# Optimization experiments

Hardware: AMD Instinct MI355X
Metric: run time of the kernel (lower is better)

The kernel has to match this reference:

```python
import jax, jax.numpy as jnp
import numpy as np

D = 1024   # dim_model
H = 16     # num_heads
DH = D // H  # per-head dim for k and v
B, S = 2, 2048
EPS = 1e-5


def layer_norm(x, g, b):
    mu = jnp.mean(x, axis=-1, keepdims=True)
    var = jnp.var(x, axis=-1, keepdims=True)
    return (x - mu) * jax.lax.rsqrt(var + EPS) * g + b


def setup_inputs() -> dict:
    key = jax.random.key(0)
    ks = jax.random.split(key, 8)
    s_d = 1.0 / np.sqrt(D)
    inp = {
        "x": jax.random.normal(ks[0], (B, S, D), dtype=jnp.float32),
        # stacked per-head projections, [H, D, DH] (torch Linear weight.T per head)
        "wq": jax.random.uniform(ks[1], (H, D, DH), jnp.float32, -s_d, s_d),
        "wk": jax.random.uniform(ks[2], (H, D, DH), jnp.float32, -s_d, s_d),
        "wv": jax.random.uniform(ks[3], (H, D, DH), jnp.float32, -s_d, s_d),
        "wo": jax.random.uniform(ks[4], (D, D), jnp.float32, -s_d, s_d),
        "w1": jax.random.uniform(ks[5], (D, D), jnp.float32, -s_d, s_d),  # FFN hidden == dim_model per source
        "w2": jax.random.uniform(ks[6], (D, D), jnp.float32, -s_d, s_d),
        "ln1_g": jnp.ones((D,), jnp.float32), "ln1_b": jnp.zeros((D,), jnp.float32),
        "ln2_g": jnp.ones((D,), jnp.float32), "ln2_b": jnp.zeros((D,), jnp.float32),
        "ln3_g": jnp.ones((D,), jnp.float32), "ln3_b": jnp.zeros((D,), jnp.float32),
    }
    return inp


def reference(x, wq, wk, wv, wo, w1, w2, ln1_g, ln1_b, ln2_g, ln2_b, ln3_g, ln3_b):
    residual = x
    h = layer_norm(x, ln1_g, ln1_b)  # pre_attention_norm
    # batched multi-head attention (equivalent to per-head loop + concat)
    q = jnp.einsum("bsd,hdk->bhsk", h, wq)
    k = jnp.einsum("bsd,hdk->bhsk", h, wk)
    v = jnp.einsum("bsd,hdk->bhsk", h, wv)
    scores = jnp.einsum("bhsk,bhtk->bhst", q, k) / jnp.sqrt(jnp.float32(DH))
    attn = jax.nn.softmax(scores, axis=-1)
    ctx = jnp.einsum("bhst,bhtk->bhsk", attn, v)        # [B,H,S,DH]
    concat = ctx.transpose(0, 2, 1, 3).reshape(x.shape[0], x.shape[1], -1)  # head concat order
    h = concat @ wo
    h = h + residual
    h = layer_norm(h, ln2_g, ln2_b)  # post_attention_norm (dropout is identity, rate=0)
    residual = h
    ffn = jnp.maximum(h @ w1, 0.0) @ w2
    h = ffn + residual
    h = layer_norm(h, ln3_g, ln3_b)  # post_ffn_norm
    return h
```

## Files before the change

kernel.cpp:

```cpp
#include <hip/hip_runtime.h>
#include <stdint.h>

typedef unsigned short u16;
typedef __attribute__((ext_vector_type(8))) short short8;
typedef __attribute__((ext_vector_type(4))) short short4v;
typedef __attribute__((ext_vector_type(4))) float f32x4;

#define DEV static __device__ __forceinline__

constexpr int DMODEL = 1024;
constexpr int SEQ = 2048;

DEV u16 f2b(float f){
  uint32_t u = __float_as_uint(f);
  u += 0x7FFF + ((u >> 16) & 1);
  return (u16)(u >> 16);
}

DEV float b2f(u16 b){ uint32_t u = ((uint32_t)b)<<16; return __uint_as_float(u); }

#define AS1(p) ((const __attribute__((address_space(1))) void*)(p))
#define AS3(p) ((__attribute__((address_space(3))) void*)(p))
#define GLOAD_LDS16(g, l) __builtin_amdgcn_global_load_lds(AS1(g), AS3(l), 16, 0, 0)
#define LDSADDR(p) ((uint32_t)(size_t)((__attribute__((address_space(3))) void*)(p)))

DEV short4v ds_tr16(uint32_t a){
  short4v r;
  asm volatile("ds_read_b64_tr_b16 %0, %1" : "=v"(r) : "v"(a) : "memory");
  return r;
}

DEV void pswap(uint32_t &a, uint32_t &b){
  asm("v_permlane32_swap_b32 %0, %1":"+v"(a),"+v"(b));
  asm("v_permlane16_swap_b32 %0, %1":"+v"(a),"+v"(b));
}

DEV uint32_t cvtpk(float lo, float hi){
  uint32_t r; asm("v_cvt_pk_bf16_f32 %0, %1, %2":"=v"(r):"v"(lo),"v"(hi)); return r;
}

__global__ __launch_bounds__(256) void transpose_all(
    const float* __restrict__ wq, const float* __restrict__ wk,
    const float* __restrict__ wv, const float* __restrict__ wo,
    const float* __restrict__ w1, const float* __restrict__ w2,
    u16* __restrict__ WqkvT, u16* __restrict__ WoT,
    u16* __restrict__ W1T, u16* __restrict__ W2T){
  __shared__ float tile[64][65];
  int bid = blockIdx.x;
  int j = threadIdx.x & 63, i0 = threadIdx.x >> 6;
  if(bid < 768){
    int xb = bid & 15, z = bid >> 4;
    int p = z >> 4, h = z & 15;
    const float* src = (p==0?wq:(p==1?wk:wv)) + (size_t)h*1024*64;
    float sc = (p==0) ? 0.18033688011112042f : 1.0f;
    int r0 = xb*64;
    for(int i=i0;i<64;i+=4) tile[i][j] = src[(size_t)(r0+i)*64 + j];
    __syncthreads();
    u16* drow = WqkvT + ((size_t)p*1024 + h*64)*1024;
    for(int jj=i0;jj<64;jj+=4) drow[(size_t)jj*1024 + r0 + j] = f2b(tile[j][jj]*sc);
  } else {
    int t = bid - 768;
    int which = t >> 8; t &= 255;
    const float* src = which==0?wo:(which==1?w1:w2);
    u16* dst = which==0?WoT:(which==1?W1T:W2T);
    int r0 = (t&15)*64, c0 = (t>>4)*64;
    for(int i=i0;i<64;i+=4) tile[i][j] = src[(size_t)(r0+i)*1024 + c0 + j];
    __syncthreads();
    for(int jj=i0;jj<64;jj+=4) dst[(size_t)(c0+jj)*1024 + r0 + j] = f2b(tile[j][jj]);
  }
}

__global__ __launch_bounds__(256) void ln_kernel(
    const float* __restrict__ in, const float* __restrict__ g, const float* __restrict__ bb,
    u16* __restrict__ outb, float* __restrict__ outf){
  int row = blockIdx.x, tid = threadIdx.x;
  const float4* x4 = (const float4*)(in + (size_t)row*DMODEL);
  float4 v = x4[tid];
  float s  = v.x+v.y+v.z+v.w;
  float ss = v.x*v.x + v.y*v.y + v.z*v.z + v.w*v.w;
  #pragma unroll
  for(int m=1;m<64;m<<=1){ s += __shfl_xor(s,m); ss += __shfl_xor(ss,m); }
  __shared__ float red[8];
  int w = tid>>6;
  if((tid&63)==0){ red[w]=s; red[4+w]=ss; }
  __syncthreads();
  s  = red[0]+red[1]+red[2]+red[3];
  ss = red[4]+red[5]+red[6]+red[7];
  float mu  = s*(1.f/DMODEL);
  float var = ss*(1.f/DMODEL) - mu*mu;
  float rs  = rsqrtf(var + 1e-5f);
  float4 gv = ((const float4*)g)[tid];
  float4 bv = ((const float4*)bb)[tid];
  float y0=(v.x-mu)*rs*gv.x+bv.x, y1=(v.y-mu)*rs*gv.y+bv.y;
  float y2=(v.z-mu)*rs*gv.z+bv.z, y3=(v.w-mu)*rs*gv.w+bv.w;
  if(outb){ ushort4 o = make_ushort4(f2b(y0),f2b(y1),f2b(y2),f2b(y3));
            ((ushort4*)outb)[(size_t)row*(DMODEL/4) + tid] = o; }
  if(outf){ ((float4*)outf)[(size_t)row*(DMODEL/4) + tid] = make_float4(y0,y1,y2,y3); }
}

__global__ __launch_bounds__(256) void ln_kernel_bf(
    const u16* __restrict__ in, const float* __restrict__ g, const float* __restrict__ bb,
    u16* __restrict__ outb, float* __restrict__ outf){
  int row = blockIdx.x, tid = threadIdx.x;
  ushort4 vb = ((const ushort4*)(in + (size_t)row*DMODEL))[tid];
  float v0=b2f(vb.x), v1=b2f(vb.y), v2=b2f(vb.z), v3=b2f(vb.w);
  float s  = v0+v1+v2+v3;
  float ss = v0*v0 + v1*v1 + v2*v2 + v3*v3;
  #pragma unroll
  for(int m=1;m<64;m<<=1){ s += __shfl_xor(s,m); ss += __shfl_xor(ss,m); }
  __shared__ float red[8];
  int w = tid>>6;
  if((tid&63)==0){ red[w]=s; red[4+w]=ss; }
  __syncthreads();
  s  = red[0]+red[1]+red[2]+red[3];
  ss = red[4]+red[5]+red[6]+red[7];
  float mu  = s*(1.f/DMODEL);
  float var = ss*(1.f/DMODEL) - mu*mu;
  float rs  = rsqrtf(var + 1e-5f);
  float4 gv = ((const float4*)g)[tid];
  float4 bv = ((const float4*)bb)[tid];
  float y0=(v0-mu)*rs*gv.x+bv.x, y1=(v1-mu)*rs*gv.y+bv.y;
  float y2=(v2-mu)*rs*gv.z+bv.z, y3=(v3-mu)*rs*gv.w+bv.w;
  if(outb){ ushort4 o = make_ushort4(f2b(y0),f2b(y1),f2b(y2),f2b(y3));
            ((ushort4*)outb)[(size_t)row*(DMODEL/4) + tid] = o; }
  if(outf){ ((float4*)outf)[(size_t)row*(DMODEL/4) + tid] = make_float4(y0,y1,y2,y3); }
}

template<int MODE>
__global__ __launch_bounds__(256) void gemm_bt(
    const u16* __restrict__ A, const u16* __restrict__ BT, int M, int N, int K,
    float* __restrict__ outf, u16* __restrict__ outb, const float* __restrict__ resf,
    const u16* __restrict__ resb,
    u16* __restrict__ oq, u16* __restrict__ ok, u16* __restrict__ ov){
  __shared__ u16 lsA[2][4096];
  __shared__ u16 lsB[2][4096];
  int n0 = blockIdx.x*128, m0 = blockIdx.y*128;
  int tid = threadIdx.x, lane = tid&63, w = tid>>6;
  int wr = w>>1, wc = w&1, rq = lane&15, hk = lane>>4;
  int o0 = tid*16, o1 = 4096 + tid*16;
  const u16* aS0 = A  + (size_t)(m0 + (o0>>6))*K + ((o0&63)>>1);
  const u16* aS1 = A  + (size_t)(m0 + (o1>>6))*K + ((o1&63)>>1);
  const u16* bS0 = BT + (size_t)(n0 + (o0>>6))*K + ((o0&63)>>1);
  const u16* bS1 = BT + (size_t)(n0 + (o1>>6))*K + ((o1&63)>>1);
  int nk = K>>5;
  f32x4 acc[4][4] = {};
  GLOAD_LDS16(aS0, &lsA[0][w*512]);
  GLOAD_LDS16(aS1, &lsA[0][2048 + w*512]);
  GLOAD_LDS16(bS0, &lsB[0][w*512]);
  GLOAD_LDS16(bS1, &lsB[0][2048 + w*512]);
  #pragma unroll 2
  for(int kt=0; kt<nk; ++kt){
    __syncthreads();
    if(kt+1 < nk){
      int nb = (kt+1)&1;
      GLOAD_LDS16(aS0 + (kt+1)*32, &lsA[nb][w*512]);
      GLOAD_LDS16(aS1 + (kt+1)*32, &lsA[nb][2048 + w*512]);
      GLOAD_LDS16(bS0 + (kt+1)*32, &lsB[nb][w*512]);
      GLOAD_LDS16(bS1 + (kt+1)*32, &lsB[nb][2048 + w*512]);
    }
    const u16* la = &lsA[kt&1][0];
    const u16* lb = &lsB[kt&1][0];
    short8 aF[4], bF[4];
    #pragma unroll
    for(int m=0;m<4;++m) aF[m] = *(const short8*)(la + (wr*64 + m*16 + rq)*32 + hk*8);
    #pragma unroll
    for(int n=0;n<4;++n) bF[n] = *(const short8*)(lb + (wc*64 + n*16 + rq)*32 + hk*8);
    __builtin_amdgcn_s_setprio(1);
    #pragma unroll
    for(int m=0;m<4;++m){
      #pragma unroll
      for(int n=0;n<4;++n)
        acc[m][n] = __builtin_amdgcn_mfma_f32_16x16x32_bf16(aF[m], bF[n], acc[m][n], 0,0,0);
    }
    __builtin_amdgcn_s_setprio(0);
  }
  #pragma unroll
  for(int m=0;m<4;++m){
    #pragma unroll
    for(int n=0;n<4;++n){
      int rb = m0 + wr*64 + m*16 + (hk<<2);
      int c  = n0 + wc*64 + n*16 + rq;
      #pragma unroll
      for(int qq=0;qq<4;++qq){
        int r = rb+qq; float val = acc[m][n][qq];
        if constexpr(MODE==1){
          int proj=c>>10, n1=c&1023, h=n1>>6, d2=n1&63;
          int b=r>>11, si=r&2047;
          u16* dst = proj==0?oq:(proj==1?ok:ov);
          dst[(((size_t)(b*16+h))*SEQ + si)*64 + d2] = f2b(val);
        } else if constexpr(MODE==2){
          outf[(size_t)r*N + c] = val + resf[(size_t)r*N + c];
        } else if constexpr(MODE==3){
          outb[(size_t)r*N + c] = f2b(val>0.f?val:0.f);
        } else if constexpr(MODE==4){
          outf[(size_t)r*N + c] = val + b2f(resb[(size_t)r*N + c]);
        } else if constexpr(MODE==5){
          outb[(size_t)r*N + c] = f2b(val + resf[(size_t)r*N + c]);
        } else if constexpr(MODE==6){
          outb[(size_t)r*N + c] = f2b(val + b2f(resb[(size_t)r*N + c]));
        } else {
          outb[(size_t)r*N + c] = f2b(val);
        }
      }
    }
  }
}

__global__ __launch_bounds__(256) void attn_kernel(
    const u16* __restrict__ q, const u16* __restrict__ k, const u16* __restrict__ v,
    u16* __restrict__ concat){
  __shared__ u16 lsK[2][4096];
  __shared__ u16 lsV[2][4096];
  int qt = blockIdx.x, bh = blockIdx.y;
  const u16* qp = q + (size_t)bh*SEQ*64;
  const u16* kp = k + (size_t)bh*SEQ*64;
  const u16* vp = v + (size_t)bh*SEQ*64;
  int tid=threadIdx.x, lane=tid&63, w=tid>>6;
  int rq = lane&15, hk = lane>>4;
  const uint32_t sw = (uint32_t)((rq&7)<<4);

  short8 aQ[2];
  {
    const u16* qrow = qp + (size_t)(qt*64 + w*16 + rq)*64 + hk*8;
    aQ[0] = *(const short8*)(qrow);
    aQ[1] = *(const short8*)(qrow + 32);
  }
  short8 bOnes;
  #pragma unroll
  for(int j=0;j<8;++j) bOnes[j] = (short)0x3F80;

  int o0 = tid*16,        kr0 = o0>>7;
  int o1 = 4096 + tid*16, kr1 = o1>>7;
  int koff0 = kr0*64 + ((((o0&127) ^ ((kr0&7)<<4)))>>1);
  int koff1 = kr1*64 + ((((o1&127) ^ ((kr1&7)<<4)))>>1);
  auto vdec = [](int c)->int{
    int t  = ((c>>5)<<2) | ((c&7)>>1);
    int d8 = (((c>>3)&3)<<1) | (c&1);
    return t*64 + d8*8;
  };
  int voff0 = vdec(tid), voff1 = vdec(256+tid);

  f32x4 accO[4] = {};
  f32x4 accL = {};

  GLOAD_LDS16(kp + koff0, &lsK[0][0   + w*512]);
  GLOAD_LDS16(kp + koff1, &lsK[0][2048+ w*512]);
  GLOAD_LDS16(vp + voff0, &lsV[0][0   + w*512]);
  GLOAD_LDS16(vp + voff1, &lsV[0][2048+ w*512]);

  int cur = 0;
  for(int kt=0; kt<SEQ/64; ++kt){
    __syncthreads();
    if(kt+1 < SEQ/64){
      int b = cur^1;
      const u16* ksrc = kp + (kt+1)*4096;
      const u16* vsrc = vp + (kt+1)*4096;
      GLOAD_LDS16(ksrc + koff0, &lsK[b][0   + w*512]);
      GLOAD_LDS16(ksrc + koff1, &lsK[b][2048+ w*512]);
      GLOAD_LDS16(vsrc + voff0, &lsV[b][0   + w*512]);
      GLOAD_LDS16(vsrc + voff1, &lsV[b][2048+ w*512]);
    }
    const char* kb = (const char*)&lsK[cur][0];
    short8 bK[4][2];
    #pragma unroll
    for(int ts=0;ts<4;++ts){
      uint32_t rb = (uint32_t)((ts*16+rq)*128);
      bK[ts][0] = *(const short8*)(kb + rb + (((uint32_t)(hk<<4)) ^ sw));
      bK[ts][1] = *(const short8*)(kb + rb + ((64u|(uint32_t)(hk<<4)) ^ sw));
    }
    f32x4 z[4];
    __builtin_amdgcn_s_setprio(1);
    #pragma unroll
    for(int ts=0;ts<4;++ts){
      f32x4 zz = {};
      zz = __builtin_amdgcn_mfma_f32_16x16x32_bf16(bK[ts][0], aQ[0], zz, 0,0,0);
      zz = __builtin_amdgcn_mfma_f32_16x16x32_bf16(bK[ts][1], aQ[1], zz, 0,0,0);
      z[ts] = zz;
    }
    __builtin_amdgcn_s_setprio(0);
    uint32_t vA = LDSADDR(&lsV[cur][0]) + (uint32_t)(hk*1024 + rq*2);
    short4v vL[2][4][2];
    #pragma unroll
    for(int kh=0;kh<2;++kh){
      #pragma unroll
      for(int ds=0;ds<4;++ds){
        vL[kh][ds][0] = ds_tr16(vA + kh*4096 + ds*128);
        vL[kh][ds][1] = ds_tr16(vA + kh*4096 + ds*128 + 512);
      }
    }
    #pragma unroll
    for(int ts=0;ts<4;++ts){
      #pragma unroll
      for(int r=0;r<4;++r)
        z[ts][r] = __builtin_exp2f(z[ts][r]);
    }
    uint32_t u00=cvtpk(z[0][0],z[0][1]), u01=cvtpk(z[0][2],z[0][3]);
    uint32_t u10=cvtpk(z[1][0],z[1][1]), u11=cvtpk(z[1][2],z[1][3]);
    uint32_t u20=cvtpk(z[2][0],z[2][1]), u21=cvtpk(z[2][2],z[2][3]);
    uint32_t u30=cvtpk(z[3][0],z[3][1]), u31=cvtpk(z[3][2],z[3][3]);
    pswap(u00,u10); pswap(u01,u11);
    pswap(u20,u30); pswap(u21,u31);
    union U8 { uint32_t d[4]; short8 v; } ap0, ap1;
    ap0.d[0]=u00; ap0.d[1]=u01; ap0.d[2]=u10; ap0.d[3]=u11;
    ap1.d[0]=u20; ap1.d[1]=u21; ap1.d[2]=u30; ap1.d[3]=u31;
    asm volatile("s_waitcnt lgkmcnt(0)" ::: "memory");
    __builtin_amdgcn_sched_barrier(0);
    __builtin_amdgcn_s_setprio(1);
    #pragma unroll
    for(int kh=0;kh<2;++kh){
      short8 aP = kh ? ap1.v : ap0.v;
      accL = __builtin_amdgcn_mfma_f32_16x16x32_bf16(aP, bOnes, accL, 0,0,0);
      #pragma unroll
      for(int ds=0;ds<4;++ds){
        short8 bV = __builtin_shufflevector(vL[kh][ds][0], vL[kh][ds][1], 0,1,2,3,4,5,6,7);
        accO[ds] = __builtin_amdgcn_mfma_f32_16x16x32_bf16(aP, bV, accO[ds], 0,0,0);
      }
    }
    __builtin_amdgcn_s_setprio(0);
    cur ^= 1;
  }
  int b = bh>>4, h = bh&15;
  #pragma unroll
  for(int r=0;r<4;++r){
    float inv = 1.f / accL[r];
    int si = qt*64 + w*16 + hk*4 + r;
    #pragma unroll
    for(int ds=0;ds<4;++ds){
      int c = h*64 + ds*16 + rq;
      concat[((size_t)b*SEQ + si)*DMODEL + c] = f2b(accO[ds][r] * inv);
    }
  }
}

extern "C" void kernel_launch(void* const* d_in, const int* in_sizes, int n_in,
                              void* d_out, int out_size, void* d_ws, size_t ws_size,
                              hipStream_t stream){
  (void)in_sizes; (void)n_in; (void)out_size; (void)ws_size;
  const float* x    = (const float*)d_in[0];
  const float* wq   = (const float*)d_in[1];
  const float* wk   = (const float*)d_in[2];
  const float* wv   = (const float*)d_in[3];
  const float* wo   = (const float*)d_in[4];
  const float* w1   = (const float*)d_in[5];
  const float* w2   = (const float*)d_in[6];
  const float* ln1g = (const float*)d_in[7];
  const float* ln1b = (const float*)d_in[8];
  const float* ln2g = (const float*)d_in[9];
  const float* ln2b = (const float*)d_in[10];
  const float* ln3g = (const float*)d_in[11];
  const float* ln3b = (const float*)d_in[12];
  float* out = (float*)d_out;

  char* ws = (char*)d_ws; size_t off = 0;
  auto alloc = [&](size_t b)->char*{ char* p = ws + off; off += (b + 255) & ~(size_t)255; return p; };
  u16*   WqkvT = (u16*)  alloc((size_t)3072*1024*2);
  u16*   WoT   = (u16*)  alloc((size_t)1024*1024*2);
  u16*   W1T   = (u16*)  alloc((size_t)1024*1024*2);
  u16*   W2T   = (u16*)  alloc((size_t)1024*1024*2);
  u16*   h1    = (u16*)  alloc((size_t)4096*1024*2);
  u16*   qb    = (u16*)  alloc((size_t)4194304*2);
  u16*   kb    = (u16*)  alloc((size_t)4194304*2);
  u16*   vb    = (u16*)  alloc((size_t)4194304*2);
  u16*   cc    = (u16*)  alloc((size_t)4096*1024*2);
  u16*   r1b   = (u16*)  alloc((size_t)4096*1024*2);
  u16*   h2b   = (u16*)  alloc((size_t)4096*1024*2);
  u16*   r2b   = (u16*)  alloc((size_t)4096*1024*2);
  u16*   ffn1  = h1;

  transpose_all<<<1536,256,0,stream>>>(wq,wk,wv,wo,w1,w2, WqkvT,WoT,W1T,W2T);

  ln_kernel<<<4096,256,0,stream>>>(x, ln1g, ln1b, h1, nullptr);
  gemm_bt<1><<<dim3(24,32),256,0,stream>>>(h1,WqkvT,4096,3072,1024,
      nullptr,nullptr,nullptr,nullptr, qb,kb,vb);
  attn_kernel<<<dim3(32,32),256,0,stream>>>(qb,kb,vb,cc);
  gemm_bt<5><<<dim3(8,32),256,0,stream>>>(cc,WoT,4096,1024,1024,
      nullptr,r1b,x,nullptr, nullptr,nullptr,nullptr);
  ln_kernel_bf<<<4096,256,0,stream>>>(r1b, ln2g, ln2b, h2b, nullptr);
  gemm_bt<3><<<dim3(8,32),256,0,stream>>>(h2b,W1T,4096,1024,1024,
      nullptr,ffn1,nullptr,nullptr, nullptr,nullptr,nullptr);
  gemm_bt<6><<<dim3(8,32),256,0,stream>>>(ffn1,W2T,4096,1024,1024,
      nullptr,r2b,nullptr,h2b, nullptr,nullptr,nullptr);
  ln_kernel_bf<<<4096,256,0,stream>>>(r2b, ln3g, ln3b, nullptr, out);
}
```

Baseline: 203.9 us.

## Double attention block query tile to 128 rows with 512 threads sharing K/V tiles

The attention kernel now runs 8 waves per block, each handling 16 query rows, so one block covers 128 queries instead of 64. Each shared K/V tile in LDS now serves twice as many queries, and each thread issues one global-to-LDS load per tensor instead of two. This halves K/V global traffic and halves the grid size. The cost is fewer blocks (512) and more waves waiting at each barrier, which could lower occupancy or add synchronisation stalls.

```diff
diff --git a/kernel.cpp b/kernel.cpp
--- a/kernel.cpp
+++ b/kernel.cpp
@@ -206,7 +206,7 @@
   }
 }
 
-__global__ __launch_bounds__(256) void attn_kernel(
+__global__ __launch_bounds__(512) void attn_kernel(
     const u16* __restrict__ q, const u16* __restrict__ k, const u16* __restrict__ v,
     u16* __restrict__ concat){
   __shared__ u16 lsK[2][4096];
@@ -221,7 +221,7 @@
 
   short8 aQ[2];
   {
-    const u16* qrow = qp + (size_t)(qt*64 + w*16 + rq)*64 + hk*8;
+    const u16* qrow = qp + (size_t)(qt*128 + w*16 + rq)*64 + hk*8;
     aQ[0] = *(const short8*)(qrow);
     aQ[1] = *(const short8*)(qrow + 32);
   }
@@ -229,36 +229,25 @@
   #pragma unroll
   for(int j=0;j<8;++j) bOnes[j] = (short)0x3F80;
 
-  int o0 = tid*16,        kr0 = o0>>7;
-  int o1 = 4096 + tid*16, kr1 = o1>>7;
-  int koff0 = kr0*64 + ((((o0&127) ^ ((kr0&7)<<4)))>>1);
-  int koff1 = kr1*64 + ((((o1&127) ^ ((kr1&7)<<4)))>>1);
-  auto vdec = [](int c)->int{
-    int t  = ((c>>5)<<2) | ((c&7)>>1);
-    int d8 = (((c>>3)&3)<<1) | (c&1);
-    return t*64 + d8*8;
-  };
-  int voff0 = vdec(tid), voff1 = vdec(256+tid);
+  int o = tid*16, kr = o>>7;
+  int koff = kr*64 + ((((o&127) ^ ((kr&7)<<4)))>>1);
+  int vt  = ((tid>>5)<<2) | ((tid&7)>>1);
+  int vd8 = (((tid>>3)&3)<<1) | (tid&1);
+  int voff = vt*64 + vd8*8;
 
   f32x4 accO[4] = {};
   f32x4 accL = {};
 
-  GLOAD_LDS16(kp + koff0, &lsK[0][0   + w*512]);
-  GLOAD_LDS16(kp + koff1, &lsK[0][2048+ w*512]);
-  GLOAD_LDS16(vp + voff0, &lsV[0][0   + w*512]);
-  GLOAD_LDS16(vp + voff1, &lsV[0][2048+ w*512]);
+  GLOAD_LDS16(kp + koff, &lsK[0][w*512]);
+  GLOAD_LDS16(vp + voff, &lsV[0][w*512]);
 
   int cur = 0;
   for(int kt=0; kt<SEQ/64; ++kt){
     __syncthreads();
     if(kt+1 < SEQ/64){
-      int b = cur^1;
-      const u16* ksrc = kp + (kt+1)*4096;
-      const u16* vsrc = vp + (kt+1)*4096;
-      GLOAD_LDS16(ksrc + koff0, &lsK[b][0   + w*512]);
-      GLOAD_LDS16(ksrc + koff1, &lsK[b][2048+ w*512]);
-      GLOAD_LDS16(vsrc + voff0, &lsV[b][0   + w*512]);
-      GLOAD_LDS16(vsrc + voff1, &lsV[b][2048+ w*512]);
+      int nb = cur^1;
+      GLOAD_LDS16(kp + (kt+1)*4096 + koff, &lsK[nb][w*512]);
+      GLOAD_LDS16(vp + (kt+1)*4096 + voff, &lsV[nb][w*512]);
     }
     const char* kb = (const char*)&lsK[cur][0];
     short8 bK[4][2];
@@ -323,7 +312,7 @@
   #pragma unroll
   for(int r=0;r<4;++r){
     float inv = 1.f / accL[r];
-    int si = qt*64 + w*16 + hk*4 + r;
+    int si = qt*128 + w*16 + hk*4 + r;
     #pragma unroll
     for(int ds=0;ds<4;++ds){
       int c = h*64 + ds*16 + rq;
@@ -372,7 +361,7 @@
   ln_kernel<<<4096,256,0,stream>>>(x, ln1g, ln1b, h1, nullptr);
   gemm_bt<1><<<dim3(24,32),256,0,stream>>>(h1,WqkvT,4096,3072,1024,
       nullptr,nullptr,nullptr,nullptr, qb,kb,vb);
-  attn_kernel<<<dim3(32,32),256,0,stream>>>(qb,kb,vb,cc);
+  attn_kernel<<<dim3(16,32),512,0,stream>>>(qb,kb,vb,cc);
   gemm_bt<5><<<dim3(8,32),256,0,stream>>>(cc,WoT,4096,1024,1024,
       nullptr,r1b,x,nullptr, nullptr,nullptr,nullptr);
   ln_kernel_bf<<<4096,256,0,stream>>>(r1b, ln2g, ln2b, h2b, nullptr);
```

After: 197.3 us. -3.2%, faster.
